# Kernel optimization log

Measured on AMD Instinct MI355X. Metric: run time of the kernel, lower is better.

The kernel has to match this reference:

```python
import jax, jax.numpy as jnp
import numpy as np

NE, NR, NT = 100000, 500, 365
DE = DR = DT = 200
P = min(DE, DR, DT)  # 200
B = 1024


def setup_inputs() -> dict:
    key = jax.random.key(0)
    ks = jax.random.split(key, 10)
    return {
        "e1_idx": jax.random.randint(ks[0], (B,), 0, NE),
        "r_idx": jax.random.randint(ks[1], (B,), 0, NR),
        "t_idx": jax.random.randint(ks[2], (B,), 0, NT),
        "E": jax.random.normal(ks[3], (NE, DE), dtype=jnp.float32),
        "R": jax.random.normal(ks[4], (NR, DR), dtype=jnp.float32),
        "T": jax.random.normal(ks[5], (NT, DT), dtype=jnp.float32),
        "F0": jax.random.uniform(ks[6], (DR, P), jnp.float32, -0.1, 0.1),
        "F1": jax.random.uniform(ks[7], (DE, P), jnp.float32, -0.1, 0.1),
        "F2": jax.random.uniform(ks[8], (DE, P), jnp.float32, -0.1, 0.1),
        "F3": jax.random.uniform(ks[9], (DT, P), jnp.float32, -0.1, 0.1),
    }


def reference(e1_idx, r_idx, t_idx, E, R, T, F0, F1, F2, F3):
    # Embedding lookups
    e1 = E[e1_idx]          # (B, de)
    r = R[r_idx]            # (B, dr)
    t = T[t_idx]            # (B, dt)
    # Factor projections into rank-P CPD space
    fr = r @ F0             # (B, P)
    fe1 = e1 @ F1           # (B, P)
    ft = t @ F3             # (B, P)
    FE = E @ F2             # (NE, P)
    # Diagonal core tensor I => the mm/bmm chain is exactly an
    # elementwise product over the rank dimension, then score vs all entities.
    x = (fr * fe1 * ft) @ FE.T  # (B, NE)
    return jax.nn.sigmoid(x)
```

## Files before the change

### kernel.cpp

```cpp
#include <hip/hip_runtime.h>

#define NE_  100000
#define NB_  1024
#define DD_  200
#define PP_  224

typedef _Float16 h8 __attribute__((ext_vector_type(8)));
typedef float    fx4 __attribute__((ext_vector_type(4)));

__device__ __forceinline__ float fast_sigmoid(float x) {
    float e = __builtin_amdgcn_exp2f(-1.44269504088896340736f * x);
    return __builtin_amdgcn_rcpf(1.0f + e);
}

__global__ __launch_bounds__(256) void prep_kernel(
    const int*   __restrict__ e1_idx, const int* __restrict__ r_idx,
    const int*   __restrict__ t_idx,
    const float* __restrict__ E, const float* __restrict__ R,
    const float* __restrict__ T,
    const float* __restrict__ F0, const float* __restrict__ F1,
    const float* __restrict__ F2, const float* __restrict__ F3,
    _Float16* __restrict__ h16, _Float16* __restrict__ F2t)
{
    const int tid = threadIdx.x;
    const int bid = blockIdx.x;
    if (bid < 128) {
        const int rb = bid * 8;
        const float* rrow[8];
        const float* erow[8];
        const float* trow[8];
        #pragma unroll
        for (int i = 0; i < 8; ++i) {
            rrow[i] = R + (size_t)r_idx[rb + i]  * DD_;
            erow[i] = E + (size_t)e1_idx[rb + i] * DD_;
            trow[i] = T + (size_t)t_idx[rb + i]  * DD_;
        }
        const int p = tid;
        float fr[8], fe[8], ft[8];
        #pragma unroll
        for (int i = 0; i < 8; ++i) { fr[i] = 0.f; fe[i] = 0.f; ft[i] = 0.f; }
        if (p < DD_) {
            for (int k = 0; k < DD_; ++k) {
                float f0 = F0[k * DD_ + p];
                float f1 = F1[k * DD_ + p];
                float f3 = F3[k * DD_ + p];
                #pragma unroll
                for (int i = 0; i < 8; ++i) {
                    fr[i] = fmaf(rrow[i][k], f0, fr[i]);
                    fe[i] = fmaf(erow[i][k], f1, fe[i]);
                    ft[i] = fmaf(trow[i][k], f3, ft[i]);
                }
            }
        }
        if (p < PP_) {
            #pragma unroll
            for (int i = 0; i < 8; ++i) {
                float v = (p < DD_) ? fr[i] * fe[i] * ft[i] : 0.0f;
                h16[(size_t)(rb + i) * PP_ + p] = (_Float16)v;
            }
        }
    } else {
        const int n0 = (bid - 128) * 28;
        for (int j = tid; j < 28 * PP_; j += 256) {
            int nl = j / PP_;
            int k  = j - nl * PP_;
            int n  = n0 + nl;
            float v = (n < DD_ && k < DD_) ? F2[k * DD_ + n] : 0.0f;
            F2t[(size_t)n * PP_ + k] = (_Float16)v;
        }
    }
}

__global__ __launch_bounds__(256) void fe_kernel(
    const float* __restrict__ E, const _Float16* __restrict__ F2t,
    _Float16* __restrict__ FE)
{
    const int tid  = threadIdx.x;
    const int w    = tid >> 6;
    const int l    = tid & 63;
    const int ln   = l & 15;
    const int quad = l >> 4;
    const int m0   = blockIdx.x * 64;

    int m = m0 + w * 16 + ln;
    if (m >= NE_) m = NE_ - 1;
    const float* erow = E + (size_t)m * DD_;

    h8 a[7];
    #pragma unroll
    for (int ks = 0; ks < 7; ++ks) {
        const int k = ks * 32 + quad * 8;
        h8 v = {(_Float16)0, (_Float16)0, (_Float16)0, (_Float16)0,
                (_Float16)0, (_Float16)0, (_Float16)0, (_Float16)0};
        if (k < DD_) {
            fx4 lo = *(const fx4*)(erow + k);
            fx4 hi = *(const fx4*)(erow + k + 4);
            v[0] = (_Float16)lo[0]; v[1] = (_Float16)lo[1];
            v[2] = (_Float16)lo[2]; v[3] = (_Float16)lo[3];
            v[4] = (_Float16)hi[0]; v[5] = (_Float16)hi[1];
            v[6] = (_Float16)hi[2]; v[7] = (_Float16)hi[3];
        }
        a[ks] = v;
    }

    const int mrb = m0 + w * 16 + quad * 4;
    #pragma unroll
    for (int nt = 0; nt < 14; ++nt) {
        fx4 acc = {0.f, 0.f, 0.f, 0.f};
        const _Float16* bp = F2t + (size_t)(nt * 16 + ln) * PP_ + quad * 8;
        #pragma unroll
        for (int ks = 0; ks < 7; ++ks) {
            h8 b = *(const h8*)(bp + ks * 32);
            acc = __builtin_amdgcn_mfma_f32_16x16x32_f16(a[ks], b, acc, 0, 0, 0);
        }
        #pragma unroll
        for (int r = 0; r < 4; ++r) {
            int mr = mrb + r;
            if (mr < NE_)
                FE[(size_t)mr * PP_ + nt * 16 + ln] = (_Float16)acc[r];
        }
    }
}

__global__ __launch_bounds__(256) void score_kernel(
    const _Float16* __restrict__ h16, const _Float16* __restrict__ FE,
    float* __restrict__ out)
{
    __shared__ __align__(16) _Float16 Alds[128 * 232];

    const int tid  = threadIdx.x;
    const int w    = tid >> 6;
    const int l    = tid & 63;
    const int ln   = l & 15;
    const int quad = l >> 4;
    const int wn   = w & 1;
    const int wm   = w >> 1;
    const int n_base = blockIdx.x * 64;

    h8 bfr[2][7];
    #pragma unroll
    for (int nt = 0; nt < 2; ++nt) {
        int n = n_base + wn * 32 + nt * 16 + ln;
        if (n >= NE_) n = NE_ - 1;
        const _Float16* bp = FE + (size_t)n * PP_ + quad * 8;
        #pragma unroll
        for (int ks = 0; ks < 7; ++ks)
            bfr[nt][ks] = *(const h8*)(bp + ks * 32);
    }

    const int ncol = n_base + wn * 32 + ln;

    for (int c = 0; c < 8; ++c) {
        __syncthreads();
        const _Float16* hsrc = h16 + (size_t)(c * 128) * PP_;
        #pragma unroll
        for (int j = 0; j < 14; ++j) {
            int idx = tid + j * 256;
            int row = idx / 28;
            int kp  = (idx - row * 28) * 8;
            *(h8*)&Alds[row * 232 + kp] = *(const h8*)(hsrc + (size_t)row * PP_ + kp);
        }
        __syncthreads();

        fx4 acc[4][2];
        #pragma unroll
        for (int mt = 0; mt < 4; ++mt)
            #pragma unroll
            for (int nt = 0; nt < 2; ++nt)
                acc[mt][nt] = (fx4){0.f, 0.f, 0.f, 0.f};

        #pragma unroll
        for (int ks = 0; ks < 7; ++ks) {
            h8 af[4];
            #pragma unroll
            for (int mt = 0; mt < 4; ++mt)
                af[mt] = *(const h8*)&Alds[(wm * 64 + mt * 16 + ln) * 232 +
                                           ks * 32 + quad * 8];
            #pragma unroll
            for (int mt = 0; mt < 4; ++mt)
                #pragma unroll
                for (int nt = 0; nt < 2; ++nt)
                    acc[mt][nt] = __builtin_amdgcn_mfma_f32_16x16x32_f16(
                        af[mt], bfr[nt][ks], acc[mt][nt], 0, 0, 0);
        }

        const int mbase = c * 128 + wm * 64 + quad * 4;
        #pragma unroll
        for (int nt = 0; nt < 2; ++nt) {
            int n = ncol + nt * 16;
            if (n < NE_) {
                #pragma unroll
                for (int mt = 0; mt < 4; ++mt) {
                    #pragma unroll
                    for (int r = 0; r < 4; ++r) {
                        int m = mbase + mt * 16 + r;
                        out[(size_t)m * NE_ + n] = fast_sigmoid(acc[mt][nt][r]);
                    }
                }
            }
        }
    }
}

extern "C" void kernel_launch(void* const* d_in, const int* in_sizes, int n_in,
                              void* d_out, int out_size, void* d_ws, size_t ws_size,
                              hipStream_t stream)
{
    const int*   e1_idx = (const int*)  d_in[0];
    const int*   r_idx  = (const int*)  d_in[1];
    const int*   t_idx  = (const int*)  d_in[2];
    const float* E      = (const float*)d_in[3];
    const float* R      = (const float*)d_in[4];
    const float* T      = (const float*)d_in[5];
    const float* F0     = (const float*)d_in[6];
    const float* F1     = (const float*)d_in[7];
    const float* F2     = (const float*)d_in[8];
    const float* F3     = (const float*)d_in[9];
    float* out = (float*)d_out;

    _Float16* FE16 = (_Float16*)d_ws;
    _Float16* h16  = FE16 + (size_t)NE_ * PP_;
    _Float16* F2t  = h16  + (size_t)NB_ * PP_;

    prep_kernel<<<136, 256, 0, stream>>>(e1_idx, r_idx, t_idx, E, R, T,
                                         F0, F1, F2, F3, h16, F2t);

    const int mblocks = (NE_ + 63) / 64;
    fe_kernel<<<mblocks, 256, 0, stream>>>(E, F2t, FE16);

    score_kernel<<<mblocks, 256, 0, stream>>>(h16, FE16, out);
}
```

Before: 691.6 us.

## Switch score kernel to 32x32x16 MFMA with 64-row batch chunks

Rewrites the score GEMM so each wave computes one 32x32 tile with the 32x32x16 f16 MFMA instead of eight 16x16x32 tiles. The A chunk in LDS shrinks from 128 to 64 rows, so the loop runs 16 chunks and launch bounds request 4 blocks per CU. The aim is lower register and LDS use for higher occupancy, and 32-column contiguous stores that coalesce better on the 400MB output. In exchange there are twice as many barriers and LDS refills, and less A-fragment reuse per wave.

```diff
diff --git a/kernel.cpp b/kernel.cpp
--- a/kernel.cpp
+++ b/kernel.cpp
@@ -5,8 +5,9 @@
 #define DD_  200
 #define PP_  224
 
-typedef _Float16 h8 __attribute__((ext_vector_type(8)));
+typedef _Float16 h8  __attribute__((ext_vector_type(8)));
 typedef float    fx4 __attribute__((ext_vector_type(4)));
+typedef float    fx16 __attribute__((ext_vector_type(16)));
 
 __device__ __forceinline__ float fast_sigmoid(float x) {
     float e = __builtin_amdgcn_exp2f(-1.44269504088896340736f * x);
@@ -122,81 +123,61 @@
     }
 }
 
-__global__ __launch_bounds__(256) void score_kernel(
+__global__ __launch_bounds__(256, 4) void score_kernel(
     const _Float16* __restrict__ h16, const _Float16* __restrict__ FE,
     float* __restrict__ out)
 {
-    __shared__ __align__(16) _Float16 Alds[128 * 232];
-
-    const int tid  = threadIdx.x;
-    const int w    = tid >> 6;
-    const int l    = tid & 63;
-    const int ln   = l & 15;
-    const int quad = l >> 4;
-    const int wn   = w & 1;
-    const int wm   = w >> 1;
-    const int n_base = blockIdx.x * 64;
-
-    h8 bfr[2][7];
-    #pragma unroll
-    for (int nt = 0; nt < 2; ++nt) {
-        int n = n_base + wn * 32 + nt * 16 + ln;
+    __shared__ __align__(16) _Float16 Alds[64 * 232];
+
+    const int tid = threadIdx.x;
+    const int w   = tid >> 6;
+    const int l   = tid & 63;
+    const int l31 = l & 31;
+    const int lh  = l >> 5;
+    const int wm  = w & 1;
+    const int wn  = w >> 1;
+    const int nb  = blockIdx.x * 64;
+
+    h8 bfr[14];
+    {
+        int n = nb + wn * 32 + l31;
         if (n >= NE_) n = NE_ - 1;
-        const _Float16* bp = FE + (size_t)n * PP_ + quad * 8;
-        #pragma unroll
-        for (int ks = 0; ks < 7; ++ks)
-            bfr[nt][ks] = *(const h8*)(bp + ks * 32);
-    }
-
-    const int ncol = n_base + wn * 32 + ln;
-
-    for (int c = 0; c < 8; ++c) {
+        const _Float16* bp = FE + (size_t)n * PP_ + lh * 8;
+        #pragma unroll
+        for (int ks = 0; ks < 14; ++ks)
+            bfr[ks] = *(const h8*)(bp + ks * 16);
+    }
+
+    const int ncol = nb + wn * 32 + l31;
+    const bool nok = (ncol < NE_);
+    const int srow = tid >> 2;
+    const int scol = (tid & 3) * 8;
+
+    for (int c = 0; c < 16; ++c) {
         __syncthreads();
-        const _Float16* hsrc = h16 + (size_t)(c * 128) * PP_;
-        #pragma unroll
-        for (int j = 0; j < 14; ++j) {
-            int idx = tid + j * 256;
-            int row = idx / 28;
-            int kp  = (idx - row * 28) * 8;
-            *(h8*)&Alds[row * 232 + kp] = *(const h8*)(hsrc + (size_t)row * PP_ + kp);
-        }
+        const _Float16* hsrc = h16 + (size_t)(c * 64) * PP_;
+        #pragma unroll
+        for (int j = 0; j < 7; ++j)
+            *(h8*)&Alds[srow * 232 + scol + j * 32] =
+                *(const h8*)(hsrc + (size_t)srow * PP_ + scol + j * 32);
         __syncthreads();
 
-        fx4 acc[4][2];
-        #pragma unroll
-        for (int mt = 0; mt < 4; ++mt)
+        fx16 acc;
+        #pragma unroll
+        for (int i = 0; i < 16; ++i) acc[i] = 0.0f;
+
+        #pragma unroll
+        for (int ks = 0; ks < 14; ++ks) {
+            h8 a = *(const h8*)&Alds[(wm * 32 + l31) * 232 + ks * 16 + lh * 8];
+            acc = __builtin_amdgcn_mfma_f32_32x32x16_f16(a, bfr[ks], acc, 0, 0, 0);
+        }
+
+        if (nok) {
+            const int mb = c * 64 + wm * 32 + lh * 4;
             #pragma unroll
-            for (int nt = 0; nt < 2; ++nt)
-                acc[mt][nt] = (fx4){0.f, 0.f, 0.f, 0.f};
-
-        #pragma unroll
-        for (int ks = 0; ks < 7; ++ks) {
-            h8 af[4];
-            #pragma unroll
-            for (int mt = 0; mt < 4; ++mt)
-                af[mt] = *(const h8*)&Alds[(wm * 64 + mt * 16 + ln) * 232 +
-                                           ks * 32 + quad * 8];
-            #pragma unroll
-            for (int mt = 0; mt < 4; ++mt)
-                #pragma unroll
-                for (int nt = 0; nt < 2; ++nt)
-                    acc[mt][nt] = __builtin_amdgcn_mfma_f32_16x16x32_f16(
-                        af[mt], bfr[nt][ks], acc[mt][nt], 0, 0, 0);
-        }
-
-        const int mbase = c * 128 + wm * 64 + quad * 4;
-        #pragma unroll
-        for (int nt = 0; nt < 2; ++nt) {
-            int n = ncol + nt * 16;
-            if (n < NE_) {
-                #pragma unroll
-                for (int mt = 0; mt < 4; ++mt) {
-                    #pragma unroll
-                    for (int r = 0; r < 4; ++r) {
-                        int m = mbase + mt * 16 + r;
-                        out[(size_t)m * NE_ + n] = fast_sigmoid(acc[mt][nt][r]);
-                    }
-                }
+            for (int r = 0; r < 16; ++r) {
+                int m = mb + (r & 3) + 8 * (r >> 2);
+                out[(size_t)m * NE_ + ncol] = fast_sigmoid(acc[r]);
             }
         }
     }
```

After: 666.3 us. 3.7% less time.
